# Kernel optimization log

Hardware: AMD Instinct MI355X
Metric: run time of the kernel (lower is better)

Reference implementation:

```python
import jax, jax.numpy as jnp
import numpy as np

V, C, H, W = 6, 256, 128, 128


def setup_inputs() -> dict:
    key = jax.random.key(0)
    ks = jax.random.split(key, 6)
    return {
        "q": jax.random.normal(ks[0], (V, C, H, W), dtype=jnp.float32),
        "k": jax.random.normal(ks[1], (V, C, H, W), dtype=jnp.float32),
        "v": jax.random.normal(ks[2], (V, C, H, W), dtype=jnp.float32),
        "Wq": jax.random.normal(ks[3], (C, C), dtype=jnp.float32) * (1.0 / np.sqrt(C)),
        "Wk": jax.random.normal(ks[4], (C, C), dtype=jnp.float32) * (1.0 / np.sqrt(C)),
        "Wv": jax.random.normal(ks[5], (C, C), dtype=jnp.float32) * (1.0 / np.sqrt(C)),
    }


def reference(q, k, v, Wq, Wk, Wv):
    # 1x1 conv (no bias) == channel GEMM: [V,C,H,W] x [O,C] -> [V,O,H,W]
    qp = jnp.einsum("vchw,oc->vohw", q, Wq)
    kp = jnp.einsum("vchw,oc->vohw", k, Wk)
    vp = jnp.einsum("vchw,oc->vohw", v, Wv)
    # elementwise q*k, sum over channels (dim=1, keepdim) -> [V,1,H,W]
    att = jnp.sum(qp * kp, axis=1, keepdims=True)
    # softmax over views (dim=0)
    att = jax.nn.softmax(att, axis=0)
    # weight values and sum over views (dim=0, keepdim) -> [1,C,H,W]
    out = jnp.sum(att * vp, axis=0, keepdims=True)
    return out
```

## Files before the change

### kernel.cpp

```cpp
#include <hip/hip_runtime.h>
#include <math.h>

#define HW 16384
#define C_DIM 256
#define V_DIM 6

typedef short bf16x8 __attribute__((ext_vector_type(8)));
typedef float f32x4 __attribute__((ext_vector_type(4)));

__device__ __forceinline__ unsigned short f2bf(float x) {
    unsigned u = __float_as_uint(x);
    u += 0x7FFFu + ((u >> 16) & 1u);
    return (unsigned short)(u >> 16);
}
__device__ __forceinline__ float bf2f(unsigned short h) {
    return __uint_as_float(((unsigned)h) << 16);
}

__global__ void compute_M_kernel(const float* __restrict__ Wq,
                                 const float* __restrict__ Wk,
                                 unsigned short* __restrict__ Mh,
                                 unsigned short* __restrict__ Ml) {
    const int i = blockIdx.x;
    const int j = threadIdx.x;
    float acc = 0.f;
    for (int o = 0; o < C_DIM; ++o)
        acc = fmaf(Wq[o * C_DIM + i], Wk[o * C_DIM + j], acc);
    unsigned short h = f2bf(acc);
    Mh[i * C_DIM + j] = h;
    Ml[i * C_DIM + j] = f2bf(acc - bf2f(h));
}

#define PT 64
#define BK 32
#define MROW 40

__global__ __launch_bounds__(256) void score_kernel(
        const float* __restrict__ q, const float* __restrict__ k,
        const unsigned short* __restrict__ Mh,
        const unsigned short* __restrict__ Ml,
        float* __restrict__ score) {
    const int tid  = threadIdx.x;
    const int lane = tid & 63;
    const int w    = tid >> 6;
    const int pt   = blockIdx.x & 255;
    const int v    = blockIdx.x >> 8;
    const int gp0  = pt * PT;

    __shared__ __align__(16) unsigned short Mh_s[C_DIM * MROW];
    __shared__ __align__(16) unsigned short Ml_s[C_DIM * MROW];
    __shared__ __align__(16) unsigned short Kh_s[PT * MROW];
    __shared__ __align__(16) unsigned short Kl_s[PT * MROW];
    __shared__ float s_red[4][PT];

    const float* kv = k + (size_t)v * C_DIM * HW + gp0;
    const float* qv = q + (size_t)v * C_DIM * HW + gp0;

    f32x4 acc[4][4];
    #pragma unroll
    for (int a = 0; a < 4; ++a)
        #pragma unroll
        for (int b = 0; b < 4; ++b)
            acc[a][b] = (f32x4){0.f, 0.f, 0.f, 0.f};

    const int ibase = w * 64;
    const int l15 = lane & 15;
    const int l4  = lane >> 4;

    for (int ks = 0; ks < C_DIM / BK; ++ks) {
        const int j0 = ks * BK;
        #pragma unroll
        for (int e = 0; e < 4; ++e) {
            int cidx = tid + 256 * e;
            int i  = cidx >> 2;
            int jb = cidx & 3;
            uint4 mh = *(const uint4*)(Mh + i * C_DIM + j0 + jb * 8);
            uint4 ml = *(const uint4*)(Ml + i * C_DIM + j0 + jb * 8);
            *(uint4*)&Mh_s[i * MROW + jb * 8] = mh;
            *(uint4*)&Ml_s[i * MROW + jb * 8] = ml;
        }
        #pragma unroll
        for (int e = 0; e < 4; ++e) {
            int pidx = tid + 256 * e;
            int p  = pidx & 63;
            int jp = pidx >> 6;
            const float* kp = kv + (size_t)(j0 + jp * 2) * HW + p;
            float x0 = kp[0];
            float x1 = kp[HW];
            unsigned short h0 = f2bf(x0), h1 = f2bf(x1);
            unsigned short lo0 = f2bf(x0 - bf2f(h0));
            unsigned short lo1 = f2bf(x1 - bf2f(h1));
            *(unsigned*)&Kh_s[p * MROW + jp * 2] = (unsigned)h0 | ((unsigned)h1 << 16);
            *(unsigned*)&Kl_s[p * MROW + jp * 2] = (unsigned)lo0 | ((unsigned)lo1 << 16);
        }
        __syncthreads();

        bf16x8 Ah[4], Al[4], Bh[4], Bl[4];
        #pragma unroll
        for (int it = 0; it < 4; ++it) {
            int ai = ibase + it * 16 + l15;
            Ah[it] = *(const bf16x8*)&Mh_s[ai * MROW + l4 * 8];
            Al[it] = *(const bf16x8*)&Ml_s[ai * MROW + l4 * 8];
        }
        #pragma unroll
        for (int jt = 0; jt < 4; ++jt) {
            int bp = jt * 16 + l15;
            Bh[jt] = *(const bf16x8*)&Kh_s[bp * MROW + l4 * 8];
            Bl[jt] = *(const bf16x8*)&Kl_s[bp * MROW + l4 * 8];
        }
        #pragma unroll
        for (int it = 0; it < 4; ++it)
            #pragma unroll
            for (int jt = 0; jt < 4; ++jt) {
                acc[it][jt] = __builtin_amdgcn_mfma_f32_16x16x32_bf16(
                                  Ah[it], Bh[jt], acc[it][jt], 0, 0, 0);
                acc[it][jt] = __builtin_amdgcn_mfma_f32_16x16x32_bf16(
                                  Ah[it], Bl[jt], acc[it][jt], 0, 0, 0);
                acc[it][jt] = __builtin_amdgcn_mfma_f32_16x16x32_bf16(
                                  Al[it], Bh[jt], acc[it][jt], 0, 0, 0);
            }
        __syncthreads();
    }

    float sp[4];
    #pragma unroll
    for (int jt = 0; jt < 4; ++jt) sp[jt] = 0.f;
    #pragma unroll
    for (int jt = 0; jt < 4; ++jt) {
        #pragma unroll
        for (int it = 0; it < 4; ++it) {
            int irow = ibase + it * 16 + l4 * 4;
            const float* qp = qv + (size_t)irow * HW + jt * 16 + l15;
            #pragma unroll
            for (int r = 0; r < 4; ++r)
                sp[jt] = fmaf(qp[(size_t)r * HW], acc[it][jt][r], sp[jt]);
        }
        sp[jt] += __shfl_xor(sp[jt], 16, 64);
        sp[jt] += __shfl_xor(sp[jt], 32, 64);
    }
    if (lane < 16) {
        #pragma unroll
        for (int jt = 0; jt < 4; ++jt)
            s_red[w][jt * 16 + lane] = sp[jt];
    }
    __syncthreads();
    if (tid < PT) {
        score[v * HW + gp0 + tid] =
            s_red[0][tid] + s_red[1][tid] + s_red[2][tid] + s_red[3][tid];
    }
}

__global__ __launch_bounds__(256) void softmax_w_kernel(float* __restrict__ score) {
    const int p = blockIdx.x * 256 + threadIdx.x;
    float s[V_DIM];
    float mx = -1e30f;
    #pragma unroll
    for (int vv = 0; vv < V_DIM; ++vv) {
        s[vv] = score[vv * HW + p];
        mx = fmaxf(mx, s[vv]);
    }
    float sum = 0.f;
    #pragma unroll
    for (int vv = 0; vv < V_DIM; ++vv) {
        s[vv] = __expf(s[vv] - mx);
        sum += s[vv];
    }
    float inv = 1.0f / sum;
    #pragma unroll
    for (int vv = 0; vv < V_DIM; ++vv)
        score[vv * HW + p] = s[vv] * inv;
}

__global__ void wsplit_kernel(const float* __restrict__ Wv,
                              unsigned short* __restrict__ Wvh,
                              unsigned short* __restrict__ Wvl) {
    const int i = blockIdx.x;
    const int j = threadIdx.x;
    float x = Wv[i * C_DIM + j];
    unsigned short h = f2bf(x);
    Wvh[i * C_DIM + j] = h;
    Wvl[i * C_DIM + j] = f2bf(x - bf2f(h));
}

__global__ __launch_bounds__(512) void out_gemm_kernel(
        const float* __restrict__ vin,
        const unsigned short* __restrict__ Wvh,
        const unsigned short* __restrict__ Wvl,
        const float* __restrict__ wsm,
        float* __restrict__ out) {
    const int tid  = threadIdx.x;
    const int lane = tid & 63;
    const int w    = tid >> 6;
    const int gp0  = blockIdx.x * PT;

    __shared__ __align__(16) unsigned short Wh_s[C_DIM * MROW];
    __shared__ __align__(16) unsigned short Wl_s[C_DIM * MROW];
    __shared__ __align__(16) unsigned short Xh_s[PT * MROW];
    __shared__ __align__(16) unsigned short Xl_s[PT * MROW];
    __shared__ float w_s[V_DIM][PT];

    if (tid < V_DIM * PT) {
        int vv = tid >> 6;
        int p  = tid & 63;
        w_s[vv][p] = wsm[vv * HW + gp0 + p];
    }

    f32x4 acc[2][4];
    #pragma unroll
    for (int a = 0; a < 2; ++a)
        #pragma unroll
        for (int b = 0; b < 4; ++b)
            acc[a][b] = (f32x4){0.f, 0.f, 0.f, 0.f};

    const int obase = w * 32;
    const int l15 = lane & 15;
    const int l4  = lane >> 4;

    for (int ks = 0; ks < C_DIM / BK; ++ks) {
        const int c0 = ks * BK;
        __syncthreads();
        #pragma unroll
        for (int e = 0; e < 2; ++e) {
            int cidx = tid + 512 * e;
            int i  = cidx >> 2;
            int jb = cidx & 3;
            uint4 wh = *(const uint4*)(Wvh + i * C_DIM + c0 + jb * 8);
            uint4 wl = *(const uint4*)(Wvl + i * C_DIM + c0 + jb * 8);
            *(uint4*)&Wh_s[i * MROW + jb * 8] = wh;
            *(uint4*)&Wl_s[i * MROW + jb * 8] = wl;
        }
        #pragma unroll
        for (int e = 0; e < 2; ++e) {
            int pidx = tid + 512 * e;
            int p  = pidx & 63;
            int jp = pidx >> 6;
            const float* vp = vin + (size_t)(c0 + jp * 2) * HW + gp0 + p;
            float x0 = 0.f, x1 = 0.f;
            #pragma unroll
            for (int vv = 0; vv < V_DIM; ++vv) {
                float wv = w_s[vv][p];
                const float* vvp = vp + (size_t)vv * C_DIM * HW;
                x0 = fmaf(wv, vvp[0], x0);
                x1 = fmaf(wv, vvp[HW], x1);
            }
            unsigned short h0 = f2bf(x0), h1 = f2bf(x1);
            unsigned short lo0 = f2bf(x0 - bf2f(h0));
            unsigned short lo1 = f2bf(x1 - bf2f(h1));
            *(unsigned*)&Xh_s[p * MROW + jp * 2] = (unsigned)h0 | ((unsigned)h1 << 16);
            *(unsigned*)&Xl_s[p * MROW + jp * 2] = (unsigned)lo0 | ((unsigned)lo1 << 16);
        }
        __syncthreads();

        bf16x8 Ah[2], Al[2], Bh[4], Bl[4];
        #pragma unroll
        for (int it = 0; it < 2; ++it) {
            int ai = obase + it * 16 + l15;
            Ah[it] = *(const bf16x8*)&Wh_s[ai * MROW + l4 * 8];
            Al[it] = *(const bf16x8*)&Wl_s[ai * MROW + l4 * 8];
        }
        #pragma unroll
        for (int jt = 0; jt < 4; ++jt) {
            int bp = jt * 16 + l15;
            Bh[jt] = *(const bf16x8*)&Xh_s[bp * MROW + l4 * 8];
            Bl[jt] = *(const bf16x8*)&Xl_s[bp * MROW + l4 * 8];
        }
        #pragma unroll
        for (int it = 0; it < 2; ++it)
            #pragma unroll
            for (int jt = 0; jt < 4; ++jt) {
                acc[it][jt] = __builtin_amdgcn_mfma_f32_16x16x32_bf16(
                                  Ah[it], Bh[jt], acc[it][jt], 0, 0, 0);
                acc[it][jt] = __builtin_amdgcn_mfma_f32_16x16x32_bf16(
                                  Ah[it], Bl[jt], acc[it][jt], 0, 0, 0);
                acc[it][jt] = __builtin_amdgcn_mfma_f32_16x16x32_bf16(
                                  Al[it], Bh[jt], acc[it][jt], 0, 0, 0);
            }
    }

    #pragma unroll
    for (int it = 0; it < 2; ++it)
        #pragma unroll
        for (int jt = 0; jt < 4; ++jt) {
            #pragma unroll
            for (int r = 0; r < 4; ++r) {
                int o = obase + it * 16 + l4 * 4 + r;
                out[(size_t)o * HW + gp0 + jt * 16 + l15] = acc[it][jt][r];
            }
        }
}

extern "C" void kernel_launch(void* const* d_in, const int* in_sizes, int n_in,
                              void* d_out, int out_size, void* d_ws, size_t ws_size,
                              hipStream_t stream) {
    const float* q  = (const float*)d_in[0];
    const float* k  = (const float*)d_in[1];
    const float* v  = (const float*)d_in[2];
    const float* Wq = (const float*)d_in[3];
    const float* Wk = (const float*)d_in[4];
    const float* Wv = (const float*)d_in[5];
    float* out = (float*)d_out;

    unsigned short* Mh = (unsigned short*)d_ws;
    unsigned short* Ml = Mh + C_DIM * C_DIM;
    float* score = (float*)(Ml + C_DIM * C_DIM);

    compute_M_kernel<<<C_DIM, C_DIM, 0, stream>>>(Wq, Wk, Mh, Ml);
    score_kernel<<<V_DIM * 256, 256, 0, stream>>>(q, k, Mh, Ml, score);
    softmax_w_kernel<<<HW / 256, 256, 0, stream>>>(score);
    wsplit_kernel<<<C_DIM, C_DIM, 0, stream>>>(Wv, Mh, Ml);
    out_gemm_kernel<<<HW / PT, 512, 0, stream>>>(v, Mh, Ml, score, out);
}
```

Measured before the change: 123.4 us.

## Double-buffer activation tiles, read weight fragments from global, truncate bf16 split

Both GEMM kernels now double-buffer the activation tile in LDS, prefetching the next K-slice into registers while MFMAs run on the current one, and use one barrier per iteration. The weight operands (M and Wv hi/lo) are no longer staged in LDS and are read directly from global/L2 as MFMA fragments. The bf16 hi/lo split switches from round-to-nearest to truncation, and compute_M uses four independent accumulators. This is meant to hide global load latency and cut LDS traffic, at the cost of more L2 fragment loads and more register pressure. Truncation changes rounding slightly.

```diff
diff --git a/kernel.cpp b/kernel.cpp
--- a/kernel.cpp
+++ b/kernel.cpp
@@ -4,17 +4,19 @@
 #define HW 16384
 #define C_DIM 256
 #define V_DIM 6
+#define PT 64
+#define BK 32
+#define KROW 40
 
 typedef short bf16x8 __attribute__((ext_vector_type(8)));
 typedef float f32x4 __attribute__((ext_vector_type(4)));
 
-__device__ __forceinline__ unsigned short f2bf(float x) {
+__device__ __forceinline__ void split2(float x, unsigned short& h,
+                                       unsigned short& l) {
     unsigned u = __float_as_uint(x);
-    u += 0x7FFFu + ((u >> 16) & 1u);
-    return (unsigned short)(u >> 16);
-}
-__device__ __forceinline__ float bf2f(unsigned short h) {
-    return __uint_as_float(((unsigned)h) << 16);
+    h = (unsigned short)(u >> 16);
+    float xl = x - __uint_as_float(u & 0xFFFF0000u);
+    l = (unsigned short)(__float_as_uint(xl) >> 16);
 }
 
 __global__ void compute_M_kernel(const float* __restrict__ Wq,
@@ -23,17 +25,20 @@
                                  unsigned short* __restrict__ Ml) {
     const int i = blockIdx.x;
     const int j = threadIdx.x;
-    float acc = 0.f;
-    for (int o = 0; o < C_DIM; ++o)
-        acc = fmaf(Wq[o * C_DIM + i], Wk[o * C_DIM + j], acc);
-    unsigned short h = f2bf(acc);
+    float a0 = 0.f, a1 = 0.f, a2 = 0.f, a3 = 0.f;
+    #pragma unroll 4
+    for (int o = 0; o < C_DIM; o += 4) {
+        a0 = fmaf(Wq[(o + 0) * C_DIM + i], Wk[(o + 0) * C_DIM + j], a0);
+        a1 = fmaf(Wq[(o + 1) * C_DIM + i], Wk[(o + 1) * C_DIM + j], a1);
+        a2 = fmaf(Wq[(o + 2) * C_DIM + i], Wk[(o + 2) * C_DIM + j], a2);
+        a3 = fmaf(Wq[(o + 3) * C_DIM + i], Wk[(o + 3) * C_DIM + j], a3);
+    }
+    float acc = (a0 + a1) + (a2 + a3);
+    unsigned short h, l;
+    split2(acc, h, l);
     Mh[i * C_DIM + j] = h;
-    Ml[i * C_DIM + j] = f2bf(acc - bf2f(h));
-}
-
-#define PT 64
-#define BK 32
-#define MROW 40
+    Ml[i * C_DIM + j] = l;
+}
 
 __global__ __launch_bounds__(256) void score_kernel(
         const float* __restrict__ q, const float* __restrict__ k,
@@ -46,11 +51,13 @@
     const int pt   = blockIdx.x & 255;
     const int v    = blockIdx.x >> 8;
     const int gp0  = pt * PT;
-
-    __shared__ __align__(16) unsigned short Mh_s[C_DIM * MROW];
-    __shared__ __align__(16) unsigned short Ml_s[C_DIM * MROW];
-    __shared__ __align__(16) unsigned short Kh_s[PT * MROW];
-    __shared__ __align__(16) unsigned short Kl_s[PT * MROW];
+    const int l15  = lane & 15;
+    const int l4   = lane >> 4;
+    const int p_s  = tid & 63;
+    const int jg   = tid >> 6;
+
+    __shared__ __align__(16) unsigned short Kh_s[2][PT * KROW];
+    __shared__ __align__(16) unsigned short Kl_s[2][PT * KROW];
     __shared__ float s_red[4][PT];
 
     const float* kv = k + (size_t)v * C_DIM * HW + gp0;
@@ -63,51 +70,56 @@
         for (int b = 0; b < 4; ++b)
             acc[a][b] = (f32x4){0.f, 0.f, 0.f, 0.f};
 
+    {
+        const float* kp = kv + (size_t)(jg * 8) * HW + p_s;
+        float x[8];
+        #pragma unroll
+        for (int e = 0; e < 8; ++e) x[e] = kp[(size_t)e * HW];
+        unsigned short h[8], l[8];
+        #pragma unroll
+        for (int e = 0; e < 8; ++e) split2(x[e], h[e], l[e]);
+        uint4 H, L;
+        H.x = (unsigned)h[0] | ((unsigned)h[1] << 16);
+        H.y = (unsigned)h[2] | ((unsigned)h[3] << 16);
+        H.z = (unsigned)h[4] | ((unsigned)h[5] << 16);
+        H.w = (unsigned)h[6] | ((unsigned)h[7] << 16);
+        L.x = (unsigned)l[0] | ((unsigned)l[1] << 16);
+        L.y = (unsigned)l[2] | ((unsigned)l[3] << 16);
+        L.z = (unsigned)l[4] | ((unsigned)l[5] << 16);
+        L.w = (unsigned)l[6] | ((unsigned)l[7] << 16);
+        *(uint4*)&Kh_s[0][p_s * KROW + jg * 8] = H;
+        *(uint4*)&Kl_s[0][p_s * KROW + jg * 8] = L;
+    }
+    __syncthreads();
+
     const int ibase = w * 64;
-    const int l15 = lane & 15;
-    const int l4  = lane >> 4;
 
     for (int ks = 0; ks < C_DIM / BK; ++ks) {
-        const int j0 = ks * BK;
-        #pragma unroll
-        for (int e = 0; e < 4; ++e) {
-            int cidx = tid + 256 * e;
-            int i  = cidx >> 2;
-            int jb = cidx & 3;
-            uint4 mh = *(const uint4*)(Mh + i * C_DIM + j0 + jb * 8);
-            uint4 ml = *(const uint4*)(Ml + i * C_DIM + j0 + jb * 8);
-            *(uint4*)&Mh_s[i * MROW + jb * 8] = mh;
-            *(uint4*)&Ml_s[i * MROW + jb * 8] = ml;
-        }
-        #pragma unroll
-        for (int e = 0; e < 4; ++e) {
-            int pidx = tid + 256 * e;
-            int p  = pidx & 63;
-            int jp = pidx >> 6;
-            const float* kp = kv + (size_t)(j0 + jp * 2) * HW + p;
-            float x0 = kp[0];
-            float x1 = kp[HW];
-            unsigned short h0 = f2bf(x0), h1 = f2bf(x1);
-            unsigned short lo0 = f2bf(x0 - bf2f(h0));
-            unsigned short lo1 = f2bf(x1 - bf2f(h1));
-            *(unsigned*)&Kh_s[p * MROW + jp * 2] = (unsigned)h0 | ((unsigned)h1 << 16);
-            *(unsigned*)&Kl_s[p * MROW + jp * 2] = (unsigned)lo0 | ((unsigned)lo1 << 16);
-        }
-        __syncthreads();
-
-        bf16x8 Ah[4], Al[4], Bh[4], Bl[4];
+        const int cur = ks & 1;
+
+        float x[8];
+        if (ks < 7) {
+            const float* kp = kv + (size_t)((ks + 1) * BK + jg * 8) * HW + p_s;
+            #pragma unroll
+            for (int e = 0; e < 8; ++e) x[e] = kp[(size_t)e * HW];
+        }
+
+        bf16x8 Ah[4], Al[4];
         #pragma unroll
         for (int it = 0; it < 4; ++it) {
-            int ai = ibase + it * 16 + l15;
-            Ah[it] = *(const bf16x8*)&Mh_s[ai * MROW + l4 * 8];
-            Al[it] = *(const bf16x8*)&Ml_s[ai * MROW + l4 * 8];
-        }
+            int row = ibase + it * 16 + l15;
+            Ah[it] = *(const bf16x8*)(Mh + (size_t)row * C_DIM + ks * BK + l4 * 8);
+            Al[it] = *(const bf16x8*)(Ml + (size_t)row * C_DIM + ks * BK + l4 * 8);
+        }
+
+        bf16x8 Bh[4], Bl[4];
         #pragma unroll
         for (int jt = 0; jt < 4; ++jt) {
             int bp = jt * 16 + l15;
-            Bh[jt] = *(const bf16x8*)&Kh_s[bp * MROW + l4 * 8];
-            Bl[jt] = *(const bf16x8*)&Kl_s[bp * MROW + l4 * 8];
-        }
+            Bh[jt] = *(const bf16x8*)&Kh_s[cur][bp * KROW + l4 * 8];
+            Bl[jt] = *(const bf16x8*)&Kl_s[cur][bp * KROW + l4 * 8];
+        }
+
         #pragma unroll
         for (int it = 0; it < 4; ++it)
             #pragma unroll
@@ -119,6 +131,23 @@
                 acc[it][jt] = __builtin_amdgcn_mfma_f32_16x16x32_bf16(
                                   Al[it], Bh[jt], acc[it][jt], 0, 0, 0);
             }
+
+        if (ks < 7) {
+            unsigned short h[8], l[8];
+            #pragma unroll
+            for (int e = 0; e < 8; ++e) split2(x[e], h[e], l[e]);
+            uint4 H, L;
+            H.x = (unsigned)h[0] | ((unsigned)h[1] << 16);
+            H.y = (unsigned)h[2] | ((unsigned)h[3] << 16);
+            H.z = (unsigned)h[4] | ((unsigned)h[5] << 16);
+            H.w = (unsigned)h[6] | ((unsigned)h[7] << 16);
+            L.x = (unsigned)l[0] | ((unsigned)l[1] << 16);
+            L.y = (unsigned)l[2] | ((unsigned)l[3] << 16);
+            L.z = (unsigned)l[4] | ((unsigned)l[5] << 16);
+            L.w = (unsigned)l[6] | ((unsigned)l[7] << 16);
+            *(uint4*)&Kh_s[cur ^ 1][p_s * KROW + jg * 8] = H;
+            *(uint4*)&Kl_s[cur ^ 1][p_s * KROW + jg * 8] = L;
+        }
         __syncthreads();
     }
 
@@ -176,10 +205,10 @@
                               unsigned short* __restrict__ Wvl) {
     const int i = blockIdx.x;
     const int j = threadIdx.x;
-    float x = Wv[i * C_DIM + j];
-    unsigned short h = f2bf(x);
+    unsigned short h, l;
+    split2(Wv[i * C_DIM + j], h, l);
     Wvh[i * C_DIM + j] = h;
-    Wvl[i * C_DIM + j] = f2bf(x - bf2f(h));
+    Wvl[i * C_DIM + j] = l;
 }
 
 __global__ __launch_bounds__(512) void out_gemm_kernel(
@@ -192,18 +221,19 @@
     const int lane = tid & 63;
     const int w    = tid >> 6;
     const int gp0  = blockIdx.x * PT;
-
-    __shared__ __align__(16) unsigned short Wh_s[C_DIM * MROW];
-    __shared__ __align__(16) unsigned short Wl_s[C_DIM * MROW];
-    __shared__ __align__(16) unsigned short Xh_s[PT * MROW];
-    __shared__ __align__(16) unsigned short Xl_s[PT * MROW];
-    __shared__ float w_s[V_DIM][PT];
-
-    if (tid < V_DIM * PT) {
-        int vv = tid >> 6;
-        int p  = tid & 63;
-        w_s[vv][p] = wsm[vv * HW + gp0 + p];
-    }
+    const int l15  = lane & 15;
+    const int l4   = lane >> 4;
+    const int p_s  = tid & 63;
+    const int jg   = tid >> 6;
+
+    __shared__ __align__(16) unsigned short Xh_s[2][PT * KROW];
+    __shared__ __align__(16) unsigned short Xl_s[2][PT * KROW];
+
+    float wr[V_DIM];
+    #pragma unroll
+    for (int vv = 0; vv < V_DIM; ++vv) wr[vv] = wsm[vv * HW + gp0 + p_s];
+
+    const float* vbase = vin + gp0 + p_s;
 
     f32x4 acc[2][4];
     #pragma unroll
@@ -212,58 +242,62 @@
         for (int b = 0; b < 4; ++b)
             acc[a][b] = (f32x4){0.f, 0.f, 0.f, 0.f};
 
+    {
+        float xv[4][V_DIM];
+        #pragma unroll
+        for (int vv = 0; vv < V_DIM; ++vv)
+            #pragma unroll
+            for (int e = 0; e < 4; ++e)
+                xv[e][vv] = vbase[(size_t)(vv * C_DIM + jg * 4 + e) * HW];
+        unsigned short h[4], l[4];
+        #pragma unroll
+        for (int e = 0; e < 4; ++e) {
+            float s = 0.f;
+            #pragma unroll
+            for (int vv = 0; vv < V_DIM; ++vv) s = fmaf(wr[vv], xv[e][vv], s);
+            split2(s, h[e], l[e]);
+        }
+        uint2 H, L;
+        H.x = (unsigned)h[0] | ((unsigned)h[1] << 16);
+        H.y = (unsigned)h[2] | ((unsigned)h[3] << 16);
+        L.x = (unsigned)l[0] | ((unsigned)l[1] << 16);
+        L.y = (unsigned)l[2] | ((unsigned)l[3] << 16);
+        *(uint2*)&Xh_s[0][p_s * KROW + jg * 4] = H;
+        *(uint2*)&Xl_s[0][p_s * KROW + jg * 4] = L;
+    }
+    __syncthreads();
+
     const int obase = w * 32;
-    const int l15 = lane & 15;
-    const int l4  = lane >> 4;
 
     for (int ks = 0; ks < C_DIM / BK; ++ks) {
-        const int c0 = ks * BK;
-        __syncthreads();
-        #pragma unroll
-        for (int e = 0; e < 2; ++e) {
-            int cidx = tid + 512 * e;
-            int i  = cidx >> 2;
-            int jb = cidx & 3;
-            uint4 wh = *(const uint4*)(Wvh + i * C_DIM + c0 + jb * 8);
-            uint4 wl = *(const uint4*)(Wvl + i * C_DIM + c0 + jb * 8);
-            *(uint4*)&Wh_s[i * MROW + jb * 8] = wh;
-            *(uint4*)&Wl_s[i * MROW + jb * 8] = wl;
-        }
-        #pragma unroll
-        for (int e = 0; e < 2; ++e) {
-            int pidx = tid + 512 * e;
-            int p  = pidx & 63;
-            int jp = pidx >> 6;
-            const float* vp = vin + (size_t)(c0 + jp * 2) * HW + gp0 + p;
-            float x0 = 0.f, x1 = 0.f;
-            #pragma unroll
-            for (int vv = 0; vv < V_DIM; ++vv) {
-                float wv = w_s[vv][p];
-                const float* vvp = vp + (size_t)vv * C_DIM * HW;
-                x0 = fmaf(wv, vvp[0], x0);
-                x1 = fmaf(wv, vvp[HW], x1);
-            }
-            unsigned short h0 = f2bf(x0), h1 = f2bf(x1);
-            unsigned short lo0 = f2bf(x0 - bf2f(h0));
-            unsigned short lo1 = f2bf(x1 - bf2f(h1));
-            *(unsigned*)&Xh_s[p * MROW + jp * 2] = (unsigned)h0 | ((unsigned)h1 << 16);
-            *(unsigned*)&Xl_s[p * MROW + jp * 2] = (unsigned)lo0 | ((unsigned)lo1 << 16);
-        }
-        __syncthreads();
-
-        bf16x8 Ah[2], Al[2], Bh[4], Bl[4];
+        const int cur = ks & 1;
+
+        float xv[4][V_DIM];
+        if (ks < 7) {
+            #pragma unroll
+            for (int vv = 0; vv < V_DIM; ++vv)
+                #pragma unroll
+                for (int e = 0; e < 4; ++e)
+                    xv[e][vv] = vbase[(size_t)(vv * C_DIM + (ks + 1) * BK +
+                                               jg * 4 + e) * HW];
+        }
+
+        bf16x8 Ah[2], Al[2];
         #pragma unroll
         for (int it = 0; it < 2; ++it) {
-            int ai = obase + it * 16 + l15;
-            Ah[it] = *(const bf16x8*)&Wh_s[ai * MROW + l4 * 8];
-            Al[it] = *(const bf16x8*)&Wl_s[ai * MROW + l4 * 8];
-        }
+            int row = obase + it * 16 + l15;
+            Ah[it] = *(const bf16x8*)(Wvh + (size_t)row * C_DIM + ks * BK + l4 * 8);
+            Al[it] = *(const bf16x8*)(Wvl + (size_t)row * C_DIM + ks * BK + l4 * 8);
+        }
+
+        bf16x8 Bh[4], Bl[4];
         #pragma unroll
         for (int jt = 0; jt < 4; ++jt) {
             int bp = jt * 16 + l15;
-            Bh[jt] = *(const bf16x8*)&Xh_s[bp * MROW + l4 * 8];
-            Bl[jt] = *(const bf16x8*)&Xl_s[bp * MROW + l4 * 8];
-        }
+            Bh[jt] = *(const bf16x8*)&Xh_s[cur][bp * KROW + l4 * 8];
+            Bl[jt] = *(const bf16x8*)&Xl_s[cur][bp * KROW + l4 * 8];
+        }
+
         #pragma unroll
         for (int it = 0; it < 2; ++it)
             #pragma unroll
@@ -275,18 +309,36 @@
                 acc[it][jt] = __builtin_amdgcn_mfma_f32_16x16x32_bf16(
                                   Al[it], Bh[jt], acc[it][jt], 0, 0, 0);
             }
+
+        if (ks < 7) {
+            unsigned short h[4], l[4];
+            #pragma unroll
+            for (int e = 0; e < 4; ++e) {
+                float s = 0.f;
+                #pragma unroll
+                for (int vv = 0; vv < V_DIM; ++vv) s = fmaf(wr[vv], xv[e][vv], s);
+                split2(s, h[e], l[e]);
+            }
+            uint2 H, L;
+            H.x = (unsigned)h[0] | ((unsigned)h[1] << 16);
+            H.y = (unsigned)h[2] | ((unsigned)h[3] << 16);
+            L.x = (unsigned)l[0] | ((unsigned)l[1] << 16);
+            L.y = (unsigned)l[2] | ((unsigned)l[3] << 16);
+            *(uint2*)&Xh_s[cur ^ 1][p_s * KROW + jg * 4] = H;
+            *(uint2*)&Xl_s[cur ^ 1][p_s * KROW + jg * 4] = L;
+        }
+        __syncthreads();
     }
 
     #pragma unroll
     for (int it = 0; it < 2; ++it)
         #pragma unroll
-        for (int jt = 0; jt < 4; ++jt) {
+        for (int jt = 0; jt < 4; ++jt)
             #pragma unroll
             for (int r = 0; r < 4; ++r) {
                 int o = obase + it * 16 + l4 * 4 + r;
                 out[(size_t)o * HW + gp0 + jt * 16 + l15] = acc[it][jt][r];
             }
-        }
 }
 
 extern "C" void kernel_launch(void* const* d_in, const int* in_sizes, int n_in,
```

Result: slower. 152.4 us (+23.5%).
